# Kernel tuning notes

Measured on AMD Instinct MI355X. Metric: run time of the kernel, lower is better.

Reference implementation:

```python
import jax, jax.numpy as jnp
import numpy as np

B, S, C = 16, 1024, 1024
E, H = 1024, 16
DH = E // H

def setup_inputs() -> dict:
    key = jax.random.key(0)
    k1, k2, k3, k4, k5 = jax.random.split(key, 5)
    x = jax.random.normal(k1, (B, S, C), dtype=jnp.float32)
    # learned params, sized per init_kwargs (torch Linear default init scale ~ 1/sqrt(fan_in))
    w_qkv = jax.random.normal(k2, (C, 3 * E), dtype=jnp.float32) / np.sqrt(C)
    b_qkv = jax.random.normal(k3, (3 * E,), dtype=jnp.float32) * 0.01
    w_o = jax.random.normal(k4, (E, E), dtype=jnp.float32) / np.sqrt(E)
    b_o = jax.random.normal(k5, (E,), dtype=jnp.float32) * 0.01
    return {"x": x, "w_qkv": w_qkv, "b_qkv": b_qkv, "w_o": w_o, "b_o": b_o}

def reference(x, w_qkv, b_qkv, w_o, b_o):
    b, s, _ = x.shape
    # fused QKV projection: [B,S,3E] -> [B,S,H,3*Dh]
    qkv = (jnp.einsum('bsc,ce->bse', x, w_qkv) + b_qkv).reshape(b, s, H, 3 * DH)
    q, k, v = jnp.split(qkv, 3, axis=-1)  # each [B,S,H,Dh]
    # NOTE: faithful to source — attention over the HEADS axis at each position,
    # scaled by embed_size**-0.5 (not head_dim).
    attn = jnp.einsum('bshd,bstd->bsht', q, k) * (E ** -0.5)  # [B,S,H,H]
    attn = jax.nn.softmax(attn, axis=-1)
    out = jnp.einsum('bsht,bstd->bshd', attn, v).reshape(b, s, E)
    return jnp.einsum('bse,ef->bsf', out, w_o) + b_o
```

## Files before the change

kernel.cpp:

```cpp
#include <hip/hip_runtime.h>
#include <hip/hip_bf16.h>
#include <stdint.h>

#define DEVINLINE __device__ __forceinline__

typedef __attribute__((ext_vector_type(4))) float f32x4;
typedef __attribute__((ext_vector_type(8))) short bf16x8;

DEVINLINE unsigned short f2bf(float f) {
    union { float f; uint32_t u; } v; v.f = f;
    uint32_t u = v.u;
    uint32_t rounding = 0x7FFFu + ((u >> 16) & 1u);
    u += rounding;
    return (unsigned short)(u >> 16);
}

DEVINLINE float bf2f(unsigned short h) {
    union { uint32_t u; float f; } v; v.u = ((uint32_t)h) << 16;
    return v.f;
}

__global__ void cvt_f32_bf16(const float* __restrict__ in,
                             unsigned short* __restrict__ out, int n) {
    int i = (blockIdx.x * blockDim.x + threadIdx.x) * 4;
    int stride = gridDim.x * blockDim.x * 4;
    for (; i < n; i += stride) {
        float4 v = *reinterpret_cast<const float4*>(in + i);
        ushort4 o;
        o.x = f2bf(v.x); o.y = f2bf(v.y); o.z = f2bf(v.z); o.w = f2bf(v.w);
        *reinterpret_cast<ushort4*>(out + i) = o;
    }
}

__global__ void transpose_cvt(const float* __restrict__ in,
                              unsigned short* __restrict__ out,
                              int R, int Ccols) {
    __shared__ float tile[32][33];
    int c0 = blockIdx.x * 32, r0 = blockIdx.y * 32;
    int tx = threadIdx.x, ty = threadIdx.y;
    #pragma unroll
    for (int j = 0; j < 32; j += 8)
        tile[ty + j][tx] = in[(size_t)(r0 + ty + j) * Ccols + c0 + tx];
    __syncthreads();
    #pragma unroll
    for (int j = 0; j < 32; j += 8)
        out[(size_t)(c0 + ty + j) * R + r0 + tx] = f2bf(tile[tx][ty + j]);
}


#define GLD(srcp, dstp) __builtin_amdgcn_global_load_lds( \
    (const __attribute__((address_space(1))) void*)(srcp), \
    (__attribute__((address_space(3))) void*)(dstp), 16, 0, 0)

#define STAGE(P, regionUS, srcBase, row0, kkE) do { \
    const unsigned short* _s = (srcBase) + (size_t)(row0) * K + (kkE); \
    unsigned short* _d = lds + (P) * 32768 + (regionUS) + wid * 512; \
    GLD(_s, _d); GLD(_s + (size_t)64 * K, _d + 4096); } while (0)

#define RD_A(dst, AS0, AS1, h) do { _Pragma("unroll") \
    for (int _i = 0; _i < 4; ++_i) { \
        dst[_i][0] = *(const bf16x8*)((AS0) + ((h) * 8192 + _i * 2048)); \
        dst[_i][1] = *(const bf16x8*)((AS1) + ((h) * 8192 + _i * 2048)); } } while (0)

#define RD_B(dst, BS0, BS1, nh) do { _Pragma("unroll") \
    for (int _j = 0; _j < 2; ++_j) { \
        dst[_j][0] = *(const bf16x8*)((BS0) + ((nh) * 4096 + _j * 2048)); \
        dst[_j][1] = *(const bf16x8*)((BS1) + ((nh) * 4096 + _j * 2048)); } } while (0)

#define MMA(aX, bY, mh, nh) do { \
    __builtin_amdgcn_s_setprio(1); \
    _Pragma("unroll") for (int _i = 0; _i < 4; ++_i) { \
    _Pragma("unroll") for (int _j = 0; _j < 2; ++_j) { \
        acc[(mh)*4+_i][(nh)*2+_j] = __builtin_amdgcn_mfma_f32_16x16x32_bf16( \
            aX[_i][0], bY[_j][0], acc[(mh)*4+_i][(nh)*2+_j], 0, 0, 0); \
        acc[(mh)*4+_i][(nh)*2+_j] = __builtin_amdgcn_mfma_f32_16x16x32_bf16( \
            aX[_i][1], bY[_j][1], acc[(mh)*4+_i][(nh)*2+_j], 0, 0, 0); } } \
    __builtin_amdgcn_s_setprio(0); } while (0)

#define VM4 asm volatile("s_waitcnt vmcnt(4)" ::: "memory")
#define BAR() asm volatile("s_barrier" ::: "memory")

#define KTILE(AS0c, AS1c, BS0c, BS1c, AS0n, AS1n, BS0n, BS1n, Pc, kk) do { \
    MMA(aA, bA, 0, 0); \
    RD_B(bB, BS0c, BS1c, 1); \
    BAR(); \
    MMA(aA, bB, 0, 1); \
    RD_A(aB, AS0c, AS1c, 1); \
    VM4; BAR(); \
    MMA(aB, bA, 1, 0); \
    RD_B(bA, BS0n, BS1n, 0); \
    STAGE(Pc, 16384, bSrc, 0,   kk); \
    STAGE(Pc, 24576, bSrc, 128, kk); \
    VM4; BAR(); \
    MMA(aB, bB, 1, 1); \
    RD_A(aA, AS0n, AS1n, 0); \
    STAGE(Pc, 0,     aSrc, 0,   kk); \
    STAGE(Pc, 8192,  aSrc, 128, kk); \
    BAR(); } while (0)

template <bool OUT_BF16>
__launch_bounds__(512, 2)
__global__ void gemm256(const unsigned short* __restrict__ A,
                        const unsigned short* __restrict__ Bt,
                        const float* __restrict__ bias,
                        void* __restrict__ Cout,
                        int M, int N, int K, int NTN) {
    __shared__ unsigned short lds[65536];
    const int NT = K >> 6;

    int t = threadIdx.x;
    int wid = t >> 6, lane = t & 63;
    int wr = wid >> 2, wc = wid & 3;
    int fr = lane & 15, fq = lane >> 4;

    int nwg = gridDim.x, bid = blockIdx.x;
    int cpx = nwg >> 3;
    int swz = (bid & 7) * cpx + (bid >> 3);
    int tm = swz / NTN, tn = swz % NTN;
    int bm = tm * 256, bn = tn * 256;

    int rowl = t >> 3, col8 = t & 7;
    int swzcol = (col8 ^ (rowl & 7)) << 3;
    const unsigned short* aSrc = A + (size_t)(bm + rowl) * K + swzcol;
    const unsigned short* bSrc = Bt + (size_t)(bn + rowl) * K + swzcol;

    int swzm = (fr & 7) << 3;
    int colS0 = (fq << 3) ^ swzm;
    int colS1 = (32 | (fq << 3)) ^ swzm;

    char* ldsb = (char*)lds;
    char* A00 = ldsb + ((wr * 128 + fr) << 7) + 2 * colS0;
    char* A10 = ldsb + ((wr * 128 + fr) << 7) + 2 * colS1;
    char* B00 = ldsb + ((256 + wc * 64 + fr) << 7) + 2 * colS0;
    char* B10 = ldsb + ((256 + wc * 64 + fr) << 7) + 2 * colS1;
    char* A01 = A00 + 65536; char* A11 = A10 + 65536;
    char* B01 = B00 + 65536; char* B11 = B10 + 65536;

    f32x4 acc[8][4] = {};
    bf16x8 aA[4][2], aB[4][2], bA[2][2], bB[2][2];

    STAGE(0, 0,     aSrc, 0,   0);
    STAGE(0, 8192,  aSrc, 128, 0);
    STAGE(0, 16384, bSrc, 0,   0);
    STAGE(0, 24576, bSrc, 128, 0);
    STAGE(1, 16384, bSrc, 0,   64);
    STAGE(1, 24576, bSrc, 128, 64);
    STAGE(1, 0,     aSrc, 0,   64);
    STAGE(1, 8192,  aSrc, 128, 64);
    asm volatile("s_waitcnt vmcnt(8)" ::: "memory");
    BAR();
    RD_A(aA, A00, A10, 0);
    RD_B(bA, B00, B10, 0);

    for (int tau = 0; tau < NT; tau += 2) {
        int kkA = ((tau + 2 < NT) ? (tau + 2) : (NT - 1)) << 6;
        KTILE(A00, A10, B00, B10, A01, A11, B01, B11, 0, kkA);
        int kkB = ((tau + 3 < NT) ? (tau + 3) : (NT - 1)) << 6;
        KTILE(A01, A11, B01, B11, A00, A10, B00, B10, 1, kkB);
    }
    asm volatile("s_waitcnt vmcnt(0)" ::: "memory");

    #pragma unroll
    for (int m = 0; m < 8; ++m) {
        #pragma unroll
        for (int n = 0; n < 4; ++n) {
            int col = bn + wc * 64 + n * 16 + fr;
            float bv = bias[col];
            #pragma unroll
            for (int r = 0; r < 4; ++r) {
                int row = bm + wr * 128 + m * 16 + fq * 4 + r;
                float v = acc[m][n][r] + bv;
                if (OUT_BF16)
                    ((unsigned short*)Cout)[(size_t)row * N + col] = f2bf(v);
                else
                    ((float*)Cout)[(size_t)row * N + col] = v;
            }
        }
    }
}

__global__ __launch_bounds__(64)
void attn_kernel(const unsigned short* __restrict__ qkv,
                 unsigned short* __restrict__ out) {
    __shared__ float sv[16][68];
    __shared__ float sp[16][17];
    int pos = blockIdx.x;
    int l = threadIdx.x;
    const unsigned short* rowp = qkv + (size_t)pos * 3072;

    #pragma unroll
    for (int j = 0; j < 4; ++j) {
        int i8 = (j * 64 + l) * 8;
        int h = i8 >> 6, d = i8 & 63;
        ushort4 v0 = *reinterpret_cast<const ushort4*>(rowp + h * 192 + 128 + d);
        ushort4 v1 = *reinterpret_cast<const ushort4*>(rowp + h * 192 + 128 + d + 4);
        sv[h][d + 0] = bf2f(v0.x); sv[h][d + 1] = bf2f(v0.y);
        sv[h][d + 2] = bf2f(v0.z); sv[h][d + 3] = bf2f(v0.w);
        sv[h][d + 4] = bf2f(v1.x); sv[h][d + 5] = bf2f(v1.y);
        sv[h][d + 6] = bf2f(v1.z); sv[h][d + 7] = bf2f(v1.w);
    }

    int fr = l & 15, fq = l >> 4;
    const unsigned short* hb = rowp + fr * 192 + fq * 8;
    bf16x8 kf0 = *reinterpret_cast<const bf16x8*>(hb + 64);
    bf16x8 kf1 = *reinterpret_cast<const bf16x8*>(hb + 96);
    bf16x8 qf0 = *reinterpret_cast<const bf16x8*>(hb);
    bf16x8 qf1 = *reinterpret_cast<const bf16x8*>(hb + 32);
    f32x4 st = {};
    st = __builtin_amdgcn_mfma_f32_16x16x32_bf16(kf0, qf0, st, 0, 0, 0);
    st = __builtin_amdgcn_mfma_f32_16x16x32_bf16(kf1, qf1, st, 0, 0, 0);

    float s0 = st[0] * 0.03125f, s1 = st[1] * 0.03125f;
    float s2 = st[2] * 0.03125f, s3 = st[3] * 0.03125f;
    float m = fmaxf(fmaxf(s0, s1), fmaxf(s2, s3));
    m = fmaxf(m, __shfl_xor(m, 16));
    m = fmaxf(m, __shfl_xor(m, 32));
    float e0 = __expf(s0 - m), e1 = __expf(s1 - m);
    float e2 = __expf(s2 - m), e3 = __expf(s3 - m);
    float sum = e0 + e1 + e2 + e3;
    sum += __shfl_xor(sum, 16);
    sum += __shfl_xor(sum, 32);
    float inv = 1.0f / sum;
    sp[fr][fq * 4 + 0] = e0 * inv;
    sp[fr][fq * 4 + 1] = e1 * inv;
    sp[fr][fq * 4 + 2] = e2 * inv;
    sp[fr][fq * 4 + 3] = e3 * inv;
    __syncthreads();

    int h2 = l >> 2, tq = l & 3;
    int dbase = tq * 16;
    float4 o0 = {}, o1 = {}, o2 = {}, o3 = {};
    #pragma unroll
    for (int tt = 0; tt < 16; ++tt) {
        float p = sp[h2][tt];
        float4 v0 = *reinterpret_cast<const float4*>(&sv[tt][dbase + 0]);
        float4 v1 = *reinterpret_cast<const float4*>(&sv[tt][dbase + 4]);
        float4 v2 = *reinterpret_cast<const float4*>(&sv[tt][dbase + 8]);
        float4 v3 = *reinterpret_cast<const float4*>(&sv[tt][dbase + 12]);
        o0.x += p * v0.x; o0.y += p * v0.y; o0.z += p * v0.z; o0.w += p * v0.w;
        o1.x += p * v1.x; o1.y += p * v1.y; o1.z += p * v1.z; o1.w += p * v1.w;
        o2.x += p * v2.x; o2.y += p * v2.y; o2.z += p * v2.z; o2.w += p * v2.w;
        o3.x += p * v3.x; o3.y += p * v3.y; o3.z += p * v3.z; o3.w += p * v3.w;
    }
    ushort4* po = (ushort4*)(out + (size_t)pos * 1024 + h2 * 64 + dbase);
    ushort4 w0 = { f2bf(o0.x), f2bf(o0.y), f2bf(o0.z), f2bf(o0.w) };
    ushort4 w1 = { f2bf(o1.x), f2bf(o1.y), f2bf(o1.z), f2bf(o1.w) };
    ushort4 w2 = { f2bf(o2.x), f2bf(o2.y), f2bf(o2.z), f2bf(o2.w) };
    ushort4 w3 = { f2bf(o3.x), f2bf(o3.y), f2bf(o3.z), f2bf(o3.w) };
    po[0] = w0; po[1] = w1; po[2] = w2; po[3] = w3;
}

extern "C" void kernel_launch(void* const* d_in, const int* in_sizes, int n_in,
                              void* d_out, int out_size, void* d_ws, size_t ws_size,
                              hipStream_t stream) {
    const float* x     = (const float*)d_in[0];
    const float* w_qkv = (const float*)d_in[1];
    const float* b_qkv = (const float*)d_in[2];
    const float* w_o   = (const float*)d_in[3];
    const float* b_o   = (const float*)d_in[4];
    float* out = (float*)d_out;

    const int C = 1024, E = 1024;
    const int M = 16 * 1024;
    const int N1 = 3 * E;

    char* ws = (char*)d_ws;
    unsigned short* xb    = (unsigned short*)ws;
    unsigned short* wqkvT = xb    + (size_t)M * C;
    unsigned short* qkv   = wqkvT + (size_t)N1 * C;
    unsigned short* woT   = qkv   + (size_t)M * N1;
    unsigned short* aout  = woT   + (size_t)E * E;

    cvt_f32_bf16<<<2048, 256, 0, stream>>>(x, xb, M * C);
    dim3 tb(32, 8);
    transpose_cvt<<<dim3(N1 / 32, C / 32), tb, 0, stream>>>(w_qkv, wqkvT, C, N1);
    transpose_cvt<<<dim3(E / 32, E / 32), tb, 0, stream>>>(w_o, woT, E, E);

    gemm256<true><<<dim3((M / 256) * (N1 / 256)), 512, 0, stream>>>(
        xb, wqkvT, b_qkv, qkv, M, N1, C, N1 / 256);
    attn_kernel<<<M, 64, 0, stream>>>(qkv, aout);
    gemm256<false><<<dim3((M / 256) * (E / 256)), 512, 0, stream>>>(
        aout, woT, b_o, out, M, E, E, E / 256);
}
```

Measured before the change: 192.1 us.

## Load GEMM B operand directly from global memory into registers, stage only A in LDS

The B tile no longer goes through LDS. Each wave reads its B fragments straight from global memory into registers, one k-tile ahead. Only the A tile is staged into LDS, with four rows per stage call, which halves LDS usage. This removes the LDS write and read traffic for B and may allow more occupancy. The cost is that global-load latency is exposed directly on the MFMA operand path, and the explicit vmcnt waits before the barriers were dropped, so B data readiness now depends on compiler-inserted waits.

```diff
diff --git a/kernel.cpp b/kernel.cpp
--- a/kernel.cpp
+++ b/kernel.cpp
@@ -52,20 +52,25 @@
     (const __attribute__((address_space(1))) void*)(srcp), \
     (__attribute__((address_space(3))) void*)(dstp), 16, 0, 0)
 
-#define STAGE(P, regionUS, srcBase, row0, kkE) do { \
-    const unsigned short* _s = (srcBase) + (size_t)(row0) * K + (kkE); \
-    unsigned short* _d = lds + (P) * 32768 + (regionUS) + wid * 512; \
-    GLD(_s, _d); GLD(_s + (size_t)64 * K, _d + 4096); } while (0)
+#define STAGE4(P, kkE) do { \
+    const unsigned short* _s = aSrc + (kkE); \
+    unsigned short* _d = lds + (P) * 16384 + wid * 512; \
+    GLD(_s, _d); \
+    GLD(_s + (size_t)64  * K, _d + 4096); \
+    GLD(_s + (size_t)128 * K, _d + 8192); \
+    GLD(_s + (size_t)192 * K, _d + 12288); } while (0)
 
 #define RD_A(dst, AS0, AS1, h) do { _Pragma("unroll") \
     for (int _i = 0; _i < 4; ++_i) { \
         dst[_i][0] = *(const bf16x8*)((AS0) + ((h) * 8192 + _i * 2048)); \
         dst[_i][1] = *(const bf16x8*)((AS1) + ((h) * 8192 + _i * 2048)); } } while (0)
 
-#define RD_B(dst, BS0, BS1, nh) do { _Pragma("unroll") \
-    for (int _j = 0; _j < 2; ++_j) { \
-        dst[_j][0] = *(const bf16x8*)((BS0) + ((nh) * 4096 + _j * 2048)); \
-        dst[_j][1] = *(const bf16x8*)((BS1) + ((nh) * 4096 + _j * 2048)); } } while (0)
+#define RDG_BA(kt) do { \
+    bA[0][0] = *(const bf16x8*)(gB00 + (kt)); bA[0][1] = *(const bf16x8*)(gB00 + (kt) + 32); \
+    bA[1][0] = *(const bf16x8*)(gB01 + (kt)); bA[1][1] = *(const bf16x8*)(gB01 + (kt) + 32); } while (0)
+#define RDG_BB(kt) do { \
+    bB[0][0] = *(const bf16x8*)(gB10 + (kt)); bB[0][1] = *(const bf16x8*)(gB10 + (kt) + 32); \
+    bB[1][0] = *(const bf16x8*)(gB11 + (kt)); bB[1][1] = *(const bf16x8*)(gB11 + (kt) + 32); } while (0)
 
 #define MMA(aX, bY, mh, nh) do { \
     __builtin_amdgcn_s_setprio(1); \
@@ -77,25 +82,21 @@
             aX[_i][1], bY[_j][1], acc[(mh)*4+_i][(nh)*2+_j], 0, 0, 0); } } \
     __builtin_amdgcn_s_setprio(0); } while (0)
 
-#define VM4 asm volatile("s_waitcnt vmcnt(4)" ::: "memory")
 #define BAR() asm volatile("s_barrier" ::: "memory")
 
-#define KTILE(AS0c, AS1c, BS0c, BS1c, AS0n, AS1n, BS0n, BS1n, Pc, kk) do { \
+#define KTILE(AS0c, AS1c, AS0n, AS1n, Pc, ktC, ktN, kkA) do { \
     MMA(aA, bA, 0, 0); \
-    RD_B(bB, BS0c, BS1c, 1); \
+    RDG_BB(ktC); \
     BAR(); \
     MMA(aA, bB, 0, 1); \
     RD_A(aB, AS0c, AS1c, 1); \
-    VM4; BAR(); \
+    BAR(); \
     MMA(aB, bA, 1, 0); \
-    RD_B(bA, BS0n, BS1n, 0); \
-    STAGE(Pc, 16384, bSrc, 0,   kk); \
-    STAGE(Pc, 24576, bSrc, 128, kk); \
-    VM4; BAR(); \
+    RDG_BA(ktN); \
+    BAR(); \
     MMA(aB, bB, 1, 1); \
     RD_A(aA, AS0n, AS1n, 0); \
-    STAGE(Pc, 0,     aSrc, 0,   kk); \
-    STAGE(Pc, 8192,  aSrc, 128, kk); \
+    STAGE4(Pc, kkA); \
     BAR(); } while (0)
 
 template <bool OUT_BF16>
@@ -105,7 +106,7 @@
                         const float* __restrict__ bias,
                         void* __restrict__ Cout,
                         int M, int N, int K, int NTN) {
-    __shared__ unsigned short lds[65536];
+    __shared__ unsigned short lds[32768];
     const int NT = K >> 6;
 
     int t = threadIdx.x;
@@ -122,7 +123,11 @@
     int rowl = t >> 3, col8 = t & 7;
     int swzcol = (col8 ^ (rowl & 7)) << 3;
     const unsigned short* aSrc = A + (size_t)(bm + rowl) * K + swzcol;
-    const unsigned short* bSrc = Bt + (size_t)(bn + rowl) * K + swzcol;
+
+    const unsigned short* gB00 = Bt + (size_t)(bn + wc * 64 + fr) * K + fq * 8;
+    const unsigned short* gB01 = gB00 + (size_t)16 * K;
+    const unsigned short* gB10 = gB00 + (size_t)32 * K;
+    const unsigned short* gB11 = gB00 + (size_t)48 * K;
 
     int swzm = (fr & 7) << 3;
     int colS0 = (fq << 3) ^ swzm;
@@ -131,32 +136,26 @@
     char* ldsb = (char*)lds;
     char* A00 = ldsb + ((wr * 128 + fr) << 7) + 2 * colS0;
     char* A10 = ldsb + ((wr * 128 + fr) << 7) + 2 * colS1;
-    char* B00 = ldsb + ((256 + wc * 64 + fr) << 7) + 2 * colS0;
-    char* B10 = ldsb + ((256 + wc * 64 + fr) << 7) + 2 * colS1;
-    char* A01 = A00 + 65536; char* A11 = A10 + 65536;
-    char* B01 = B00 + 65536; char* B11 = B10 + 65536;
+    char* A01 = A00 + 32768;
+    char* A11 = A10 + 32768;
 
     f32x4 acc[8][4] = {};
     bf16x8 aA[4][2], aB[4][2], bA[2][2], bB[2][2];
 
-    STAGE(0, 0,     aSrc, 0,   0);
-    STAGE(0, 8192,  aSrc, 128, 0);
-    STAGE(0, 16384, bSrc, 0,   0);
-    STAGE(0, 24576, bSrc, 128, 0);
-    STAGE(1, 16384, bSrc, 0,   64);
-    STAGE(1, 24576, bSrc, 128, 64);
-    STAGE(1, 0,     aSrc, 0,   64);
-    STAGE(1, 8192,  aSrc, 128, 64);
-    asm volatile("s_waitcnt vmcnt(8)" ::: "memory");
+    RDG_BA(0);
+    STAGE4(0, 0);
+    STAGE4(1, 64);
+    asm volatile("s_waitcnt vmcnt(4)" ::: "memory");
     BAR();
     RD_A(aA, A00, A10, 0);
-    RD_B(bA, B00, B10, 0);
 
     for (int tau = 0; tau < NT; tau += 2) {
-        int kkA = ((tau + 2 < NT) ? (tau + 2) : (NT - 1)) << 6;
-        KTILE(A00, A10, B00, B10, A01, A11, B01, B11, 0, kkA);
-        int kkB = ((tau + 3 < NT) ? (tau + 3) : (NT - 1)) << 6;
-        KTILE(A01, A11, B01, B11, A00, A10, B00, B10, 1, kkB);
+        int kt0 = tau << 6;
+        int kt1 = (tau + 1) << 6;
+        int kt2 = ((tau + 2 < NT) ? (tau + 2) : (NT - 1)) << 6;
+        int kt3 = ((tau + 3 < NT) ? (tau + 3) : (NT - 1)) << 6;
+        KTILE(A00, A10, A01, A11, 0, kt0, kt1, kt2);
+        KTILE(A01, A11, A00, A10, 1, kt1, kt2, kt3);
     }
     asm volatile("s_waitcnt vmcnt(0)" ::: "memory");
 
```

After: 267.2 us. +39.1%, slower.
